# Kernel optimization log

Measured on AMD Instinct MI355X. Metric: run time of the kernel, lower is better.

## Reference

```python
import jax, jax.numpy as jnp
import numpy as np
from jax import lax

CORRKS = 7
EPS_CORR = 1e-6
EPS_IN = 1e-5
FLOW_SCALE = 1.0


def _gauss_kernel2d():
    # kornia get_gaussian_kernel1d(7, 1.5), separable -> outer product
    x = np.arange(7, dtype=np.float32) - 3.0
    g = np.exp(-(x ** 2) / (2.0 * 1.5 ** 2))
    g = g / g.sum()
    return jnp.asarray(np.outer(g, g), dtype=jnp.float32)  # [7,7]


def conv2d(x, w, b=None, padding=1, dilation=1, groups=1):
    y = lax.conv_general_dilated(
        x, w, window_strides=(1, 1),
        padding=[(padding, padding), (padding, padding)],
        rhs_dilation=(dilation, dilation),
        dimension_numbers=("NCHW", "OIHW", "NCHW"),
        feature_group_count=groups)
    if b is not None:
        y = y + b[None, :, None, None]
    return y


def gaussian_blur(x):
    # replicate padding then depthwise 7x7 gaussian conv
    c = x.shape[1]
    k2 = _gauss_kernel2d()
    w = jnp.broadcast_to(k2[None, None], (c, 1, 7, 7))
    xp = jnp.pad(x, ((0, 0), (0, 0), (3, 3), (3, 3)), mode="edge")
    return conv2d(xp, w, padding=0, groups=c)


def instance_norm(x, gamma, beta):
    mu = x.mean(axis=(2, 3), keepdims=True)
    var = x.var(axis=(2, 3), keepdims=True)
    xn = (x - mu) * lax.rsqrt(var + EPS_IN)
    return xn * gamma[None, :, None, None] + beta[None, :, None, None]


def lrelu(x):
    return jnp.where(x >= 0, x, 0.2 * x)


def nan0(x):
    return jnp.nan_to_num(x, nan=0.0, posinf=0.0, neginf=0.0)


def setup_inputs() -> dict:
    key = jax.random.key(0)
    ks = jax.random.split(key, 20)
    b, c, h, w = 4, 64, 256, 256

    def rn(k, shape, scale):
        return jax.random.normal(k, shape, dtype=jnp.float32) * scale

    d = {}
    d["feat1"] = rn(ks[0], (b, c, h, w), 1.0)
    d["feat2"] = rn(ks[1], (b, c, h, w), 1.0)
    # preprocessor: Conv(c, c, 3, pad=1), bias, no norm/act
    d["pre_w"] = rn(ks[2], (c, c, 3, 3), 0.05)
    d["pre_b"] = jnp.zeros((c,), jnp.float32)
    # featcompressor layer1: Conv(2c,2c,3), IN affine + LeakyReLU (no bias)
    d["fc1_w"] = rn(ks[3], (2 * c, 2 * c, 3, 3), 0.05)
    d["fc1_g"] = jnp.ones((2 * c,), jnp.float32)
    d["fc1_be"] = jnp.zeros((2 * c,), jnp.float32)
    # featcompressor layer2: Conv(2c,c,3), bias, no norm/act
    d["fc2_w"] = rn(ks[4], (c, 2 * c, 3, 3), 0.05)
    d["fc2_b"] = jnp.zeros((c,), jnp.float32)
    # estimator: (c+49)->64 d1, 64->32 d2, 32->16 d4; IN + LeakyReLU, no bias
    d["e1_w"] = rn(ks[5], (64, c + CORRKS * CORRKS, 3, 3), 0.05)
    d["e1_g"] = jnp.ones((64,), jnp.float32)
    d["e1_be"] = jnp.zeros((64,), jnp.float32)
    d["e2_w"] = rn(ks[6], (32, 64, 3, 3), 0.05)
    d["e2_g"] = jnp.ones((32,), jnp.float32)
    d["e2_be"] = jnp.zeros((32,), jnp.float32)
    d["e3_w"] = rn(ks[7], (16, 32, 3, 3), 0.05)
    d["e3_g"] = jnp.ones((16,), jnp.float32)
    d["e3_be"] = jnp.zeros((16,), jnp.float32)
    # flow head (torch zero-inits; use small random so output is non-degenerate)
    d["head_w"] = rn(ks[8], (2, 16, 3, 3), 0.05)
    d["head_b"] = jnp.zeros((2,), jnp.float32)
    return d


def reference(feat1, feat2, pre_w, pre_b, fc1_w, fc1_g, fc1_be, fc2_w, fc2_b,
              e1_w, e1_g, e1_be, e2_w, e2_g, e2_be, e3_w, e3_g, e3_be,
              head_w, head_b):
    # preprocessor applied to both features (cat on batch == apply separately)
    f1 = conv2d(feat1, pre_w, pre_b, padding=1)
    f2 = conv2d(feat2, pre_w, pre_b, padding=1)

    # featcompressor
    feat = conv2d(jnp.concatenate([f1, f2], axis=1), fc1_w, padding=1)
    feat = lrelu(instance_norm(feat, fc1_g, fc1_be))
    feat = conv2d(feat, fc2_w, fc2_b, padding=1)

    # local correlation: (feat2 - shifted blurred feat1)^2 mean over channels
    b, c, h, w = f2.shape
    f1s = gaussian_blur(f1)
    pad = CORRKS // 2  # corr_dilation=1
    f1p = jnp.pad(f1s, ((0, 0), (0, 0), (pad, pad), (pad, pad)))  # zero pad (F.unfold)
    lc = jnp.stack(
        [((f2 - f1p[:, :, i:i + h, j:j + w]) ** 2).mean(axis=1)
         for i in range(CORRKS) for j in range(CORRKS)], axis=1)  # [b,49,h,w]
    lc = lc / (lc.mean(axis=(1, 2, 3), keepdims=True) + EPS_CORR)
    corr = nan0(jnp.concatenate([feat, lc], axis=1))  # [b, c+49, h, w]

    # dilated conv estimator stack
    x = lrelu(instance_norm(conv2d(corr, e1_w, padding=1, dilation=1), e1_g, e1_be))
    x = lrelu(instance_norm(conv2d(x, e2_w, padding=2, dilation=2), e2_g, e2_be))
    x = lrelu(instance_norm(conv2d(x, e3_w, padding=4, dilation=4), e3_g, e3_be))

    disp = conv2d(x, head_w, head_b, padding=1) * FLOW_SCALE
    disp = nan0(gaussian_blur(disp))
    return disp
```

## Files before the change

### kernel.cpp

```cpp
#include <hip/hip_runtime.h>
#include <hip/hip_bf16.h>


typedef __attribute__((ext_vector_type(8))) short short8;
typedef __attribute__((ext_vector_type(4))) float f32x4;
typedef _Float16 f16x8 __attribute__((ext_vector_type(8)));

__device__ __forceinline__ float s2f(short s) {
    unsigned int u = ((unsigned int)(unsigned short)s) << 16;
    float f; __builtin_memcpy(&f, &u, 4); return f;
}
__device__ __forceinline__ short f2s(float f) {
    __hip_bfloat16 h = __float2bfloat16(f);
    short s; __builtin_memcpy(&s, &h, 2); return s;
}
__device__ __forceinline__ short f2h(float f) {
    _Float16 h = (_Float16)f;
    short s; __builtin_memcpy(&s, &h, 2); return s;
}

__device__ __forceinline__ float gw(int j) {
    const float G[7] = {0.0366329f, 0.1112808f, 0.2167453f, 0.2706821f,
                        0.2167453f, 0.1112808f, 0.0366329f};
    return G[j];
}

__global__ __launch_bounds__(256) void transpose_k(const float* __restrict__ in,
                                                   short* __restrict__ out)
{
    __shared__ float t[64][65];
    const int b = blockIdx.y;
    const int px0 = blockIdx.x * 64;
    #pragma unroll
    for (int k = 0; k < 16; ++k) {
        int idx = threadIdx.x + k * 256;
        int c = idx >> 6, x = idx & 63;
        t[c][x] = in[(size_t)(b * 64 + c) * 65536 + px0 + x];
    }
    __syncthreads();
    #pragma unroll
    for (int k = 0; k < 16; ++k) {
        int idx = threadIdx.x + k * 256;
        int px = idx >> 6, c = idx & 63;
        out[(size_t)(b * 65536 + px0 + px) * 64 + c] = f2s(t[c][px]);
    }
}

__global__ __launch_bounds__(256) void repack2_k(const float* __restrict__ w,
                                                 short* __restrict__ o,
                                                 int cout, int cin, int CINP)
{
    int idx = blockIdx.x * 256 + threadIdx.x;
    int CB = CINP >> 5;
    int tot = cout * 9 * CINP;
    if (idx >= tot) return;
    int c8   = idx & 7;
    int lane = (idx >> 3) & 63;
    int rest = idx >> 9;
    int cb   = rest % CB;
    int rest2 = rest / CB;
    int tap  = rest2 % 9;
    int o16  = rest2 / 9;
    int n16 = lane & 15, q = lane >> 4;
    int oc = o16 * 16 + n16;
    int ic = cb * 32 + q * 8 + c8;
    float v = (ic < cin) ? w[(size_t)(oc * cin + ic) * 9 + tap] : 0.f;
    o[idx] = f2s(v);
}

template<int DIL, int CINP, int WX, int WY, int NOC, int G, int MODE>
__global__ __launch_bounds__(256) void convmfma_k(
    const short* __restrict__ srcA, const short* __restrict__ srcB,
    int splitK, int csA, int csB,
    const short* __restrict__ wgt, const float* __restrict__ bias,
    short* __restrict__ out, int OSTR, int OBASE, int b0,
    const float* __restrict__ xf)
{
    static_assert(WX * WY == 4, "4 waves per block");
    constexpr int PXW = G * 16;
    constexpr int PXB = PXW * WX;
    constexpr int XT  = 256 / PXB;
    constexpr int CB  = CINP / 32;
    constexpr int UQ  = CINP / 8;
    constexpr int UPX = UQ + 1;
    constexpr int WPX = PXB + 2 * DIL;

    __shared__ __align__(16) short lds[WPX * UPX * 8];

    const int tid  = threadIdx.x;
    const int lane = tid & 63;
    const int wave = tid >> 6;
    const int q = lane >> 4, n16 = lane & 15;
    const int wx = wave % WX, wy = wave / WX;

    constexpr int NX = XT * 256;
    const int bx = blockIdx.x;
    const int xs = (bx & 7) * (NX >> 3) + (bx >> 3);
    const int xt = xs % XT;
    const int y  = xs / XT;

    const int b  = b0 + blockIdx.z;
    const int ocWaveBase = blockIdx.y * (16 * NOC * WY) + wy * (16 * NOC);
    const int o16base = ocWaveBase >> 4;
    const int x0 = xt * PXB + wx * PXW;
    const int gxbase = xt * PXB - DIL;

    const int bC = b * CINP;
    const float sc = (MODE == 2) ? 1.f / (xf[b] * (1.f / 3211264.f) + 1e-6f) : 0.f;

    f32x4 acc[G][NOC];
    #pragma unroll
    for (int g = 0; g < G; ++g)
        #pragma unroll
        for (int t = 0; t < NOC; ++t)
            acc[g][t] = {0.f, 0.f, 0.f, 0.f};

    for (int dyi = 0; dyi < 3; ++dyi) {
        const int yy = y + (dyi - 1) * DIL;
        const bool rowok = ((unsigned)yy < 256u);
        __syncthreads();
        if (rowok) {
            const int rowbase = (b * 256 + yy) * 256;
            for (int i = tid; i < WPX * UQ; i += 256) {
                const int pxl = i / UQ;
                const int u   = i - pxl * UQ;
                const int gx  = gxbase + pxl;
                short8 v = {0, 0, 0, 0, 0, 0, 0, 0};
                if ((unsigned)gx < 256u) {
                    const int ic = u * 8;
                    const short* p = (ic < splitK)
                        ? srcA + (size_t)(rowbase + gx) * csA + ic
                        : srcB + (size_t)(rowbase + gx) * csB + (ic - splitK);
                    v = *reinterpret_cast<const short8*>(p);
                    if (MODE == 1) {
                        #pragma unroll
                        for (int c = 0; c < 8; ++c) {
                            const float ka = xf[2 * (bC + ic + c)];
                            const float kb = xf[2 * (bC + ic + c) + 1];
                            float t = s2f(v[c]) * ka + kb;
                            t = fmaxf(t, 0.2f * t);
                            v[c] = f2s(t);
                        }
                    } else if (MODE == 2) {
                        if (ic >= splitK) {
                            #pragma unroll
                            for (int c = 0; c < 8; ++c)
                                v[c] = f2s(s2f(v[c]) * sc);
                        }
                    }
                }
                *reinterpret_cast<short8*>(&lds[(pxl * UPX + u) * 8]) = v;
            }
        }
        __syncthreads();
        if (!rowok) continue;

        #pragma unroll
        for (int dxi = 0; dxi < 3; ++dxi) {
            const int tap = dyi * 3 + dxi;
            #pragma unroll
            for (int cb = 0; cb < CB; ++cb) {
                short8 bfr[G];
                #pragma unroll
                for (int g = 0; g < G; ++g) {
                    const int pxl = wx * PXW + g * 16 + n16 + dxi * DIL;
                    bfr[g] = *reinterpret_cast<const short8*>(
                        &lds[(pxl * UPX + cb * 4 + q) * 8]);
                }
                #pragma unroll
                for (int t = 0; t < NOC; ++t) {
                    short8 a = *reinterpret_cast<const short8*>(
                        wgt + ((((size_t)(o16base + t) * 9 + tap) * CB + cb) * 64 + lane) * 8);
                    #pragma unroll
                    for (int g = 0; g < G; ++g)
                        acc[g][t] = __builtin_amdgcn_mfma_f32_16x16x32_bf16(
                            a, bfr[g], acc[g][t], 0, 0, 0);
                }
            }
        }
    }

    #pragma unroll
    for (int g = 0; g < G; ++g) {
        const size_t px_lin = (size_t)(b * 256 + y) * 256 + x0 + g * 16 + n16;
        #pragma unroll
        for (int t = 0; t < NOC; ++t) {
            const int oc = ocWaveBase + t * 16 + q * 4;
            f32x4 v = acc[g][t];
            if (bias) {
                v.x += bias[oc];     v.y += bias[oc + 1];
                v.z += bias[oc + 2]; v.w += bias[oc + 3];
            }
            ushort4 pk;
            pk.x = (unsigned short)f2s(v.x);
            pk.y = (unsigned short)f2s(v.y);
            pk.z = (unsigned short)f2s(v.z);
            pk.w = (unsigned short)f2s(v.w);
            *reinterpret_cast<ushort4*>(out + px_lin * OSTR + OBASE + oc) = pk;
        }
    }
}

__global__ __launch_bounds__(256) void in_stats_nhwc_k(const short* __restrict__ x,
                                                       float* __restrict__ sums,
                                                       int C, int lC)
{
    __shared__ float ls[256], lss[256];
    const int tid = threadIdx.x;
    const int b = blockIdx.y;
    const int c = tid & (C - 1);
    const int sub = tid >> lC;
    const int tpc = 256 >> lC;
    const int px0 = blockIdx.x * 512;
    float s = 0.f, ss = 0.f;
    for (int p = sub; p < 512; p += tpc) {
        float v = s2f(x[(size_t)(b * 65536 + px0 + p) * C + c]);
        s += v; ss += v * v;
    }
    ls[tid] = s; lss[tid] = ss;
    __syncthreads();
    if (tid < C) {
        float s0 = ls[tid], ss0 = lss[tid];
        for (int j = 1; j < tpc; ++j) { s0 += ls[tid + j * C]; ss0 += lss[tid + j * C]; }
        atomicAdd(sums + 2 * (b * C + tid), s0);
        atomicAdd(sums + 2 * (b * C + tid) + 1, ss0);
    }
}

__global__ __launch_bounds__(256) void in_finalize_k(const float* __restrict__ sums,
                                                     float* __restrict__ stats,
                                                     const float* __restrict__ gamma,
                                                     const float* __restrict__ beta,
                                                     int lC, int n)
{
    int i = blockIdx.x * 256 + threadIdx.x;
    if (i >= n) return;
    int c = i & ((1 << lC) - 1);
    float m = sums[2 * i] * (1.f / 65536.f);
    float var = sums[2 * i + 1] * (1.f / 65536.f) - m * m;
    if (var < 0.f) var = 0.f;
    float ka = rsqrtf(var + 1e-5f) * gamma[c];
    stats[2 * i] = ka;
    stats[2 * i + 1] = beta[c] - m * ka;
}

__global__ __launch_bounds__(256) void blur_k(const short* __restrict__ A,
                                              short* __restrict__ B1)
{
    __shared__ __align__(16) short raw[484 * 8];
    __shared__ __align__(16) float hb[352 * 12];

    const int tid  = threadIdx.x;
    const int tile = blockIdx.x >> 3;
    const int g    = blockIdx.x & 7;
    const int c0   = g * 8;
    const int tx = (tile & 15) << 4;
    const int ty = (tile >> 4) << 4;
    const int b  = blockIdx.y;

    #pragma unroll
    for (int it = 0; it < 2; ++it) {
        int i = tid + it * 256;
        if (i < 484) {
            int y = i / 22, x = i - y * 22;
            int gy = ty + y - 3, gx = tx + x - 3;
            gy = gy < 0 ? 0 : (gy > 255 ? 255 : gy);
            gx = gx < 0 ? 0 : (gx > 255 ? 255 : gx);
            *reinterpret_cast<short8*>(&raw[i * 8]) =
                *reinterpret_cast<const short8*>(
                    &A[(size_t)((b << 16) + (gy << 8) + gx) * 128 + c0]);
        }
    }
    __syncthreads();

    #pragma unroll
    for (int it = 0; it < 2; ++it) {
        int i = tid + it * 256;
        if (i < 352) {
            int r = i >> 4, cc = i & 15;
            float s[8];
            #pragma unroll
            for (int c = 0; c < 8; ++c) s[c] = 0.f;
            #pragma unroll
            for (int j = 0; j < 7; ++j) {
                short8 v = *reinterpret_cast<const short8*>(&raw[(r * 22 + cc + j) * 8]);
                float w = gw(j);
                #pragma unroll
                for (int c = 0; c < 8; ++c) s[c] += w * s2f(v[c]);
            }
            #pragma unroll
            for (int c = 0; c < 8; ++c) hb[i * 12 + c] = s[c];
        }
    }
    __syncthreads();

    const int py = tid >> 4, px = tid & 15;
    float s[8];
    #pragma unroll
    for (int c = 0; c < 8; ++c) s[c] = 0.f;
    #pragma unroll
    for (int j = 0; j < 7; ++j) {
        const float* hp = &hb[((py + j) * 16 + px) * 12];
        float w = gw(j);
        #pragma unroll
        for (int c = 0; c < 8; ++c) s[c] += w * hp[c];
    }
    short8 ov;
    #pragma unroll
    for (int c = 0; c < 8; ++c) ov[c] = f2h(s[c]);
    *reinterpret_cast<short8*>(
        &B1[(size_t)(((g * 4 + b) << 16) + ((ty + py) << 8) + tx + px) * 8]) = ov;
}

__global__ __launch_bounds__(256, 2) void corr2_k(const short* __restrict__ A,
                                                  const short* __restrict__ B1,
                                                  short* __restrict__ lcPad,
                                                  float* __restrict__ lcsum)
{
    __shared__ __align__(16) short blh[2][22 * 24 * 8];
    __shared__ float red[4];

    const int tid = threadIdx.x;
    const int tx = (blockIdx.x & 15) << 4;
    const int ty = (blockIdx.x >> 4) << 4;
    const int b  = blockIdx.y;
    const int py = tid >> 4, px = tid & 15;

    int y0 = tid / 22, x0c = tid - y0 * 22;
    int gy0 = ty + y0 - 3, gx0 = tx + x0c - 3;
    const bool ok0 = (gy0 >= 0 && gy0 < 256 && gx0 >= 0 && gx0 < 256);
    gy0 = gy0 < 0 ? 0 : (gy0 > 255 ? 255 : gy0);
    gx0 = gx0 < 0 ? 0 : (gx0 > 255 ? 255 : gx0);
    const int off0 = (gy0 << 8) + gx0;
    const int lc0 = y0 * 24 + x0c;

    const int c1 = tid + 256;
    int y1 = c1 / 22, x1c = c1 - y1 * 22;
    int gy1 = ty + y1 - 3, gx1 = tx + x1c - 3;
    const bool ok1 = (gy1 >= 0 && gy1 < 256 && gx1 >= 0 && gx1 < 256);
    gy1 = gy1 < 0 ? 0 : (gy1 > 255 ? 255 : gy1);
    gx1 = gx1 < 0 ? 0 : (gx1 > 255 ? 255 : gx1);
    const int off1 = (gy1 << 8) + gx1;
    const int lc1 = y1 * 24 + x1c;
    const bool has1 = (c1 < 484);

    const short* f2p = &A[(size_t)((b << 16) + ((ty + py) << 8) + tx + px) * 128 + 64];

    float acc[49];
    #pragma unroll
    for (int k = 0; k < 49; ++k) acc[k] = 0.f;

    for (int g = 0; g < 8; ++g) {
        const size_t plane = (size_t)(g * 4 + b) << 16;
        short* buf = blh[g & 1];

        {
            short8 v = *reinterpret_cast<const short8*>(&B1[(plane + off0) * 8]);
            if (!ok0) v = v ^ v;
            *reinterpret_cast<short8*>(&buf[lc0 * 8]) = v;
            if (has1) {
                short8 w = *reinterpret_cast<const short8*>(&B1[(plane + off1) * 8]);
                if (!ok1) w = w ^ w;
                *reinterpret_cast<short8*>(&buf[lc1 * 8]) = w;
            }
        }

        short8 f2raw = *reinterpret_cast<const short8*>(f2p + g * 8);
        f16x8 f2v;
        #pragma unroll
        for (int c = 0; c < 8; ++c) f2v[c] = (_Float16)s2f(f2raw[c]);

        __syncthreads();

        const short* blp = &buf[(py * 24 + px) * 8];
        #pragma unroll
        for (int i = 0; i < 7; ++i)
            #pragma unroll
            for (int j = 0; j < 7; ++j) {
                f16x8 bv = *reinterpret_cast<const f16x8*>(blp + (i * 24 + j) * 8);
                f16x8 d = f2v - bv;
                float a = acc[i * 7 + j];
#if __has_builtin(__builtin_amdgcn_fdot2)
                a = __builtin_amdgcn_fdot2(__builtin_shufflevector(d, d, 0, 1),
                                           __builtin_shufflevector(d, d, 0, 1), a, false);
                a = __builtin_amdgcn_fdot2(__builtin_shufflevector(d, d, 2, 3),
                                           __builtin_shufflevector(d, d, 2, 3), a, false);
                a = __builtin_amdgcn_fdot2(__builtin_shufflevector(d, d, 4, 5),
                                           __builtin_shufflevector(d, d, 4, 5), a, false);
                a = __builtin_amdgcn_fdot2(__builtin_shufflevector(d, d, 6, 7),
                                           __builtin_shufflevector(d, d, 6, 7), a, false);
#else
                #pragma unroll
                for (int c = 0; c < 8; ++c) {
                    float df = (float)d[c];
                    a += df * df;
                }
#endif
                acc[i * 7 + j] = a;
            }
        __syncthreads();
    }

    const size_t base = (size_t)((b << 16) + ((ty + py) << 8) + tx + px) * 64;
    float tot = 0.f;
    #pragma unroll
    for (int k = 0; k < 49; ++k) {
        float m = acc[k] * (1.f / 64.f);
        lcPad[base + k] = f2s(m);
        tot += m;
    }
    #pragma unroll
    for (int k = 49; k < 64; ++k) lcPad[base + k] = 0;

    for (int o = 32; o; o >>= 1) tot += __shfl_down(tot, o);
    if ((tid & 63) == 0) red[tid >> 6] = tot;
    __syncthreads();
    if (tid == 0) atomicAdd(lcsum + b, red[0] + red[1] + red[2] + red[3]);
}

__global__ __launch_bounds__(256) void head_k(const short* __restrict__ e3,
                                              const float* __restrict__ w,
                                              const float* __restrict__ bias,
                                              const float* __restrict__ kst,
                                              float* __restrict__ hd)
{
    int pix = blockIdx.x * 256 + threadIdx.x;
    int b = pix >> 16, rem = pix & 65535;
    int y = rem >> 8, x = rem & 255;
    float ka[16], kb[16];
    #pragma unroll
    for (int ic = 0; ic < 16; ++ic) {
        ka[ic] = kst[2 * (b * 16 + ic)];
        kb[ic] = kst[2 * (b * 16 + ic) + 1];
    }
    float a0 = bias[0], a1 = bias[1];
    #pragma unroll
    for (int tap = 0; tap < 9; ++tap) {
        int yy = y + tap / 3 - 1, xx = x + tap % 3 - 1;
        if ((unsigned)yy >= 256u || (unsigned)xx >= 256u) continue;
        const short* p = e3 + (size_t)((b << 16) + (yy << 8) + xx) * 16;
        #pragma unroll
        for (int ic = 0; ic < 16; ++ic) {
            float v = s2f(p[ic]) * ka[ic] + kb[ic];
            v = fmaxf(v, 0.2f * v);
            a0 += v * w[ic * 9 + tap];
            a1 += v * w[(16 + ic) * 9 + tap];
        }
    }
    hd[(size_t)(b * 2) * 65536 + rem]     = a0;
    hd[(size_t)(b * 2 + 1) * 65536 + rem] = a1;
}

__global__ __launch_bounds__(256) void blur7f_k(const float* __restrict__ in,
                                                float* __restrict__ out)
{
    __shared__ float raw[22 * 22];
    __shared__ float hb[22 * 16];
    const int tid = threadIdx.x;
    const int tx = (blockIdx.x & 15) << 4;
    const int ty = (blockIdx.x >> 4) << 4;
    const size_t ch = ((size_t)blockIdx.y) << 16;
    const int py = tid >> 4, px = tid & 15;

    for (int i = tid; i < 484; i += 256) {
        int y = i / 22, x = i - y * 22;
        int gy = ty + y - 3, gx = tx + x - 3;
        gy = gy < 0 ? 0 : (gy > 255 ? 255 : gy);
        gx = gx < 0 ? 0 : (gx > 255 ? 255 : gx);
        raw[i] = in[ch + (gy << 8) + gx];
    }
    __syncthreads();
    for (int i = tid; i < 352; i += 256) {
        int r = i >> 4, cc = i & 15;
        float s = 0.f;
        #pragma unroll
        for (int j = 0; j < 7; ++j) s += gw(j) * raw[r * 22 + cc + j];
        hb[i] = s;
    }
    __syncthreads();
    float s = 0.f;
    #pragma unroll
    for (int j = 0; j < 7; ++j) s += gw(j) * hb[(py + j) * 16 + px];
    out[ch + ((ty + py) << 8) + tx + px] = s;
}

extern "C" void kernel_launch(void* const* d_in, const int* in_sizes, int n_in,
                              void* d_out, int out_size, void* d_ws, size_t ws_size,
                              hipStream_t stream)
{
    const float* feat1  = (const float*)d_in[0];
    const float* feat2  = (const float*)d_in[1];
    const float* pre_w  = (const float*)d_in[2];
    const float* pre_b  = (const float*)d_in[3];
    const float* fc1_w  = (const float*)d_in[4];
    const float* fc1_g  = (const float*)d_in[5];
    const float* fc1_be = (const float*)d_in[6];
    const float* fc2_w  = (const float*)d_in[7];
    const float* fc2_b  = (const float*)d_in[8];
    const float* e1_w   = (const float*)d_in[9];
    const float* e1_g   = (const float*)d_in[10];
    const float* e1_be  = (const float*)d_in[11];
    const float* e2_w   = (const float*)d_in[12];
    const float* e2_g   = (const float*)d_in[13];
    const float* e2_be  = (const float*)d_in[14];
    const float* e3_w   = (const float*)d_in[15];
    const float* e3_g   = (const float*)d_in[16];
    const float* e3_be  = (const float*)d_in[17];
    const float* head_w = (const float*)d_in[18];
    const float* head_b = (const float*)d_in[19];
    float* out = (float*)d_out;

    const size_t NEED = 152000000;
    if (ws_size < NEED) return;

    char* ws = (char*)d_ws;
    short* T1      = (short*)(ws);
    short* T2      = (short*)(ws + 33554432);
    short* lcPad   = (short*)(ws);
    short* B1h     = (short*)(ws + 33554432);
    short* featBuf = (short*)(ws + 33554432);
    short* A       = (short*)(ws + 67108864);
    short* FC1o    = (short*)(ws + 83886080);
    short* E1o     = (short*)(ws + 67108864);
    short* E2o     = (short*)(ws + 100663296);
    short* E3o     = (short*)(ws + 117440512);
    float* HD      = (float*)(ws + 125829120);
    short* preW    = (short*)(ws + 150994944);
    short* fc1W    = (short*)(ws + 151068672);
    short* fc2W    = (short*)(ws + 151363584);
    short* e1W     = (short*)(ws + 151511040);
    short* e2W     = (short*)(ws + 151658496);
    short* e3W     = (short*)(ws + 151695360);
    float* sums0   = (float*)(ws + 151704576);
    float* sums1   = (float*)(ws + 151708672);
    float* sums2   = (float*)(ws + 151712768);
    float* sums3   = (float*)(ws + 151716864);
    float* stats0  = (float*)(ws + 151720960);
    float* stats1  = (float*)(ws + 151725056);
    float* stats2  = (float*)(ws + 151729152);
    float* stats3  = (float*)(ws + 151733248);
    float* LS      = (float*)(ws + 151737344);

    hipMemsetAsync(ws + 151704576, 0, 32784, stream);

    transpose_k<<<dim3(1024, 4), 256, 0, stream>>>(feat1, T1);
    transpose_k<<<dim3(1024, 4), 256, 0, stream>>>(feat2, T2);

    repack2_k<<<144, 256, 0, stream>>>(pre_w, preW, 64, 64, 64);
    repack2_k<<<576, 256, 0, stream>>>(fc1_w, fc1W, 128, 128, 128);
    repack2_k<<<288, 256, 0, stream>>>(fc2_w, fc2W, 64, 128, 128);
    repack2_k<<<288, 256, 0, stream>>>(e1_w, e1W, 64, 113, 128);
    repack2_k<<<72, 256, 0, stream>>>(e2_w, e2W, 32, 64, 64);
    repack2_k<<<18, 256, 0, stream>>>(e3_w, e3W, 16, 32, 32);

    convmfma_k<1, 64, 2, 2, 2, 4, 0><<<dim3(512, 1, 4), 256, 0, stream>>>(
        T1, T1, 64, 64, 64, preW, pre_b, A, 128, 0, 0, nullptr);
    convmfma_k<1, 64, 2, 2, 2, 4, 0><<<dim3(512, 1, 4), 256, 0, stream>>>(
        T2, T2, 64, 64, 64, preW, pre_b, A, 128, 64, 0, nullptr);

    blur_k<<<dim3(2048, 4), 256, 0, stream>>>(A, B1h);
    corr2_k<<<dim3(256, 4), 256, 0, stream>>>(A, B1h, lcPad, LS);

    for (int b = 3; b >= 0; --b)
        convmfma_k<1, 128, 2, 2, 4, 4, 0><<<dim3(512, 1, 1), 256, 0, stream>>>(
            A, A, 128, 128, 128, fc1W, nullptr, FC1o, 128, 0, b, nullptr);
    in_stats_nhwc_k<<<dim3(128, 4), 256, 0, stream>>>(FC1o, sums0, 128, 7);
    in_finalize_k<<<2, 256, 0, stream>>>(sums0, stats0, fc1_g, fc1_be, 7, 512);

    convmfma_k<1, 128, 2, 2, 2, 4, 1><<<dim3(512, 1, 4), 256, 0, stream>>>(
        FC1o, FC1o, 128, 128, 128, fc2W, fc2_b, featBuf, 64, 0, 0, stats0);

    convmfma_k<1, 128, 2, 2, 2, 4, 2><<<dim3(512, 1, 4), 256, 0, stream>>>(
        featBuf, lcPad, 64, 64, 64, e1W, nullptr, E1o, 64, 0, 0, LS);
    in_stats_nhwc_k<<<dim3(128, 4), 256, 0, stream>>>(E1o, sums1, 64, 6);
    in_finalize_k<<<1, 256, 0, stream>>>(sums1, stats1, e1_g, e1_be, 6, 256);

    convmfma_k<2, 64, 2, 2, 1, 4, 1><<<dim3(512, 1, 4), 256, 0, stream>>>(
        E1o, E1o, 64, 64, 64, e2W, nullptr, E2o, 32, 0, 0, stats1);
    in_stats_nhwc_k<<<dim3(128, 4), 256, 0, stream>>>(E2o, sums2, 32, 5);
    in_finalize_k<<<1, 256, 0, stream>>>(sums2, stats2, e2_g, e2_be, 5, 128);

    convmfma_k<4, 32, 4, 1, 1, 4, 1><<<dim3(256, 1, 4), 256, 0, stream>>>(
        E2o, E2o, 32, 32, 32, e3W, nullptr, E3o, 16, 0, 0, stats2);
    in_stats_nhwc_k<<<dim3(128, 4), 256, 0, stream>>>(E3o, sums3, 16, 4);
    in_finalize_k<<<1, 256, 0, stream>>>(sums3, stats3, e3_g, e3_be, 4, 64);

    head_k<<<1024, 256, 0, stream>>>(E3o, head_w, head_b, stats3, HD);
    blur7f_k<<<dim3(256, 8), 256, 0, stream>>>(HD, out);
}
```

Before: 965.6 us.

## Prefetch next input row into registers while computing current row in conv kernel

The conv MFMA kernel now splits the LDS fill into an issue phase, which loads the next row's global data into registers, and a commit phase, which applies the transform and writes to LDS. The next row's loads are issued before the current row's MFMA compute so global latency overlaps with math. The fc1 conv launch also switches to half the pixel group size with twice the blocks. The trade-off is extra registers for the staging buffers, which may lower occupancy.

```diff
diff --git a/kernel.cpp b/kernel.cpp
--- a/kernel.cpp
+++ b/kernel.cpp
@@ -82,8 +82,12 @@
     constexpr int XT  = 256 / PXB;
     constexpr int CB  = CINP / 32;
     constexpr int UQ  = CINP / 8;
+    constexpr int LUQ = (UQ == 16) ? 4 : ((UQ == 8) ? 3 : 2);
+    static_assert(UQ == (1 << LUQ), "UQ must be 4/8/16");
     constexpr int UPX = UQ + 1;
     constexpr int WPX = PXB + 2 * DIL;
+    constexpr int NTOT = WPX * UQ;
+    constexpr int NIT  = (NTOT + 255) / 256;
 
     __shared__ __align__(16) short lds[WPX * UPX * 8];
 
@@ -108,31 +112,42 @@
     const int bC = b * CINP;
     const float sc = (MODE == 2) ? 1.f / (xf[b] * (1.f / 3211264.f) + 1e-6f) : 0.f;
 
-    f32x4 acc[G][NOC];
-    #pragma unroll
-    for (int g = 0; g < G; ++g)
-        #pragma unroll
-        for (int t = 0; t < NOC; ++t)
-            acc[g][t] = {0.f, 0.f, 0.f, 0.f};
-
-    for (int dyi = 0; dyi < 3; ++dyi) {
-        const int yy = y + (dyi - 1) * DIL;
-        const bool rowok = ((unsigned)yy < 256u);
-        __syncthreads();
-        if (rowok) {
-            const int rowbase = (b * 256 + yy) * 256;
-            for (int i = tid; i < WPX * UQ; i += 256) {
-                const int pxl = i / UQ;
-                const int u   = i - pxl * UQ;
+    short8 stg[NIT];
+
+    auto issue = [&](int yy) {
+        const int rowbase = (b * 256 + yy) * 256;
+        #pragma unroll
+        for (int it = 0; it < NIT; ++it) {
+            const int i = tid + it * 256;
+            short8 v = {0, 0, 0, 0, 0, 0, 0, 0};
+            if (i < NTOT) {
+                const int pxl = i >> LUQ;
+                const int u   = i & (UQ - 1);
                 const int gx  = gxbase + pxl;
-                short8 v = {0, 0, 0, 0, 0, 0, 0, 0};
                 if ((unsigned)gx < 256u) {
                     const int ic = u * 8;
                     const short* p = (ic < splitK)
                         ? srcA + (size_t)(rowbase + gx) * csA + ic
                         : srcB + (size_t)(rowbase + gx) * csB + (ic - splitK);
                     v = *reinterpret_cast<const short8*>(p);
-                    if (MODE == 1) {
+                }
+            }
+            stg[it] = v;
+        }
+    };
+
+    auto commit = [&]() {
+        #pragma unroll
+        for (int it = 0; it < NIT; ++it) {
+            const int i = tid + it * 256;
+            if (i < NTOT) {
+                const int pxl = i >> LUQ;
+                const int u   = i & (UQ - 1);
+                short8 v = stg[it];
+                if (MODE == 1) {
+                    const int gx = gxbase + pxl;
+                    if ((unsigned)gx < 256u) {
+                        const int ic = u * 8;
                         #pragma unroll
                         for (int c = 0; c < 8; ++c) {
                             const float ka = xf[2 * (bC + ic + c)];
@@ -141,18 +156,43 @@
                             t = fmaxf(t, 0.2f * t);
                             v[c] = f2s(t);
                         }
-                    } else if (MODE == 2) {
-                        if (ic >= splitK) {
-                            #pragma unroll
-                            for (int c = 0; c < 8; ++c)
-                                v[c] = f2s(s2f(v[c]) * sc);
-                        }
+                    }
+                } else if (MODE == 2) {
+                    const int gx = gxbase + pxl;
+                    const int ic = u * 8;
+                    if ((unsigned)gx < 256u && ic >= splitK) {
+                        #pragma unroll
+                        for (int c = 0; c < 8; ++c)
+                            v[c] = f2s(s2f(v[c]) * sc);
                     }
                 }
                 *reinterpret_cast<short8*>(&lds[(pxl * UPX + u) * 8]) = v;
             }
         }
+    };
+
+    f32x4 acc[G][NOC];
+    #pragma unroll
+    for (int g = 0; g < G; ++g)
+        #pragma unroll
+        for (int t = 0; t < NOC; ++t)
+            acc[g][t] = {0.f, 0.f, 0.f, 0.f};
+
+    {
+        const int yy0 = y - DIL;
+        if ((unsigned)yy0 < 256u) issue(yy0);
+    }
+
+    for (int dyi = 0; dyi < 3; ++dyi) {
+        const int yy = y + (dyi - 1) * DIL;
+        const bool rowok = ((unsigned)yy < 256u);
         __syncthreads();
+        if (rowok) commit();
+        __syncthreads();
+        if (dyi < 2) {
+            const int yn = y + dyi * DIL;
+            if ((unsigned)yn < 256u) issue(yn);
+        }
         if (!rowok) continue;
 
         #pragma unroll
@@ -562,7 +602,7 @@
     corr2_k<<<dim3(256, 4), 256, 0, stream>>>(A, B1h, lcPad, LS);
 
     for (int b = 3; b >= 0; --b)
-        convmfma_k<1, 128, 2, 2, 4, 4, 0><<<dim3(512, 1, 1), 256, 0, stream>>>(
+        convmfma_k<1, 128, 2, 2, 4, 2, 0><<<dim3(1024, 1, 1), 256, 0, stream>>>(
             A, A, 128, 128, 128, fc1W, nullptr, FC1o, 128, 0, b, nullptr);
     in_stats_nhwc_k<<<dim3(128, 4), 256, 0, stream>>>(FC1o, sums0, 128, 7);
     in_finalize_k<<<2, 256, 0, stream>>>(sums0, stats0, fc1_g, fc1_be, 7, 512);
```

New measurement: 910.5 us. 5.7% less time.
